# Kernel optimization log

Hardware: AMD Instinct MI355X
Metric: run time of the kernel (lower is better)

The kernel has to match this reference:

```python
import jax, jax.numpy as jnp
import numpy as np

B, D, L, H = 512, 512, 32, 300  # batch, input_dim, latent_dim, hidden_dim


def setup_inputs() -> dict:
    key = jax.random.key(0)
    ks = jax.random.split(key, 16)
    s = lambda k, *sh: jax.random.normal(k, sh, dtype=jnp.float32) * 0.05
    return {
        "x": jax.random.normal(ks[0], (B, D), dtype=jnp.float32),
        "eps": jax.random.normal(ks[1], (B, L), dtype=jnp.float32),
        "W": jax.random.normal(ks[2], (D, L), dtype=jnp.float32),  # mask (get_generator_mask -> W)
        "qz_w1": s(ks[3], D, H), "qz_b1": s(ks[4], H),
        "qz_w2": s(ks[5], H, H), "qz_b2": s(ks[6], H),
        "zm_w": s(ks[7], H, L), "zm_b": s(ks[8], L),
        "zl_w": s(ks[9], H, L), "zl_b": s(ks[10], L),
        "gen_w1": s(ks[11], L, H),               # no bias (bias=False)
        "gen_w2": s(ks[12], H, H), "gen_b2": s(ks[13], H),
        "col_w": s(ks[14], D, H), "col_b": s(ks[15], D),  # stacked column_means Linears
    }


def reference(x, eps, W, qz_w1, qz_b1, qz_w2, qz_b2, zm_w, zm_b, zl_w, zl_b,
              gen_w1, gen_w2, gen_b2, col_w, col_b):
    # encode
    h = jax.nn.relu(x @ qz_w1 + qz_b1)
    h = jax.nn.relu(h @ qz_w2 + qz_b2)
    z_mean = h @ zm_w + zm_b
    z_log_var = h @ zl_w + zl_b
    # reparameterize (eps supplied as input)
    z = z_mean + eps * jnp.exp(0.5 * z_log_var)
    # decode: per-column masked generator MLP, batched over columns j
    masked = W[:, None, :] * z[None, :, :]                 # [D, B, L]
    g = jax.nn.relu(jnp.einsum('jbl,lh->jbh', masked, gen_w1))
    g = jax.nn.relu(jnp.einsum('jbh,hk->jbk', g, gen_w2) + gen_b2)
    x_rec = jnp.einsum('jbh,jh->jb', g, col_w) + col_b[:, None]  # [D, B]
    x_mean = x_rec.T                                       # [B, D]
    return (x_mean, z, z_mean, z_log_var)
```

## Files before the change

### kernel.cpp

```cpp
#include <hip/hip_runtime.h>

#define B_ 512
#define D_ 512
#define L_ 32
#define H_ 300
#define NT 19
#define NS 10
#define G1S 308

typedef unsigned short ushort_t;
typedef __bf16 bf16x8 __attribute__((ext_vector_type(8)));
typedef float f32x4 __attribute__((ext_vector_type(4)));

union B8 { ushort_t u[8]; uint4 q; bf16x8 v; uint2 d[2]; __bf16 b[8]; };

__device__ __forceinline__ void split8(const float* fv, B8& hi, B8& lo) {
    #pragma unroll
    for (int i = 0; i < 8; ++i) {
        __bf16 h = (__bf16)fv[i];
        hi.b[i] = h;
        lo.b[i] = (__bf16)(fv[i] - (float)h);
    }
}

__global__ __launch_bounds__(64) void prep_kernel(
        const float* __restrict__ gw1, const float* __restrict__ gw2,
        const float* __restrict__ qw1, const float* __restrict__ qw2,
        const float* __restrict__ zmw, const float* __restrict__ zlw,
        ushort_t* __restrict__ gw1f, ushort_t* __restrict__ gw2f,
        ushort_t* __restrict__ w1hi, ushort_t* __restrict__ w1lo,
        ushort_t* __restrict__ w2hi, ushort_t* __restrict__ w2lo,
        ushort_t* __restrict__ w3hi, ushort_t* __restrict__ w3lo) {
    int blk = blockIdx.x;
    int l = threadIdx.x, grp = l >> 4, li = l & 15;
    if (blk < 209) {
        const float* src; int K, nt, s; ushort_t* dst;
        if (blk < 19) { nt = blk; s = 0; src = gw1; K = 32; dst = gw1f + (nt * 64 + l) * 8; }
        else { int i = blk - 19; nt = i / 10; s = i % 10; src = gw2; K = 300;
               dst = gw2f + ((nt * 10 + s) * 64 + l) * 8; }
        int n = nt * 16 + li;
        B8 V;
        #pragma unroll
        for (int i = 0; i < 8; ++i) {
            int k = 32 * s + 8 * grp + i;
            V.b[i] = (__bf16)((k < K && n < H_) ? src[k * H_ + n] : 0.f);
        }
        *reinterpret_cast<uint4*>(dst) = V.q;
    } else {
        const float* src = nullptr; int K, N, nt, s, stacked = 0;
        ushort_t *dh, *dl;
        if (blk < 513)      { int i = blk - 209; nt = i / 16; s = i % 16; src = qw1; K = 512; N = 300;
                              dh = w1hi + ((nt * 16 + s) * 64 + l) * 8; dl = w1lo + ((nt * 16 + s) * 64 + l) * 8; }
        else if (blk < 703) { int i = blk - 513; nt = i / 10; s = i % 10; src = qw2; K = 300; N = 300;
                              dh = w2hi + ((nt * 10 + s) * 64 + l) * 8; dl = w2lo + ((nt * 10 + s) * 64 + l) * 8; }
        else                { int i = blk - 703; nt = i / 10; s = i % 10; K = 300; N = 64; stacked = 1;
                              dh = w3hi + ((nt * 10 + s) * 64 + l) * 8; dl = w3lo + ((nt * 10 + s) * 64 + l) * 8; }
        int n = nt * 16 + li;
        float fv[8];
        #pragma unroll
        for (int i = 0; i < 8; ++i) {
            int k = 32 * s + 8 * grp + i;
            float v = 0.f;
            if (k < K && n < N) {
                if (!stacked) v = src[k * N + n];
                else          v = (n < 32) ? zmw[k * 32 + n] : zlw[k * 32 + (n - 32)];
            }
            fv[i] = v;
        }
        B8 Vh, Vl;
        split8(fv, Vh, Vl);
        *reinterpret_cast<uint4*>(dh) = Vh.q;
        *reinterpret_cast<uint4*>(dl) = Vl.q;
    }
}

template<int KSTEPS, bool RELU>
__global__ __launch_bounds__(256) void enc_gemm_f32(const float* __restrict__ A, int lda,
        const ushort_t* __restrict__ Whi, const ushort_t* __restrict__ Wlo,
        const float* __restrict__ bias, float* __restrict__ out, int ldo,
        int Ncols, int ntiles) {
    const int tid = threadIdx.x;
    const int w = tid >> 6, lane = tid & 63;
    const int grp = lane >> 4, li = lane & 15;
    const int r0 = blockIdx.x * 16;
    const int nt = blockIdx.y * 4 + w;
    const bool active = nt < ntiles;

    f32x4 acc = {0.f, 0.f, 0.f, 0.f};
    for (int s = 0; s < KSTEPS; ++s) {
        int kb = 32 * s + 8 * grp;
        B8 Ah, Al;
        if (kb + 8 <= lda) {
            const float* ap = A + (size_t)(r0 + li) * lda + kb;
            float4 f0 = *reinterpret_cast<const float4*>(ap);
            float4 f1 = *reinterpret_cast<const float4*>(ap + 4);
            float fv[8] = {f0.x, f0.y, f0.z, f0.w, f1.x, f1.y, f1.z, f1.w};
            split8(fv, Ah, Al);
        } else {
            Ah.q = make_uint4(0, 0, 0, 0);
            Al.q = make_uint4(0, 0, 0, 0);
        }
        if (active) {
            bf16x8 bh = *reinterpret_cast<const bf16x8*>(
                Whi + ((size_t)(nt * KSTEPS + s) * 64 + lane) * 8);
            bf16x8 bl = *reinterpret_cast<const bf16x8*>(
                Wlo + ((size_t)(nt * KSTEPS + s) * 64 + lane) * 8);
            acc = __builtin_amdgcn_mfma_f32_16x16x32_bf16(Ah.v, bh, acc, 0, 0, 0);
            acc = __builtin_amdgcn_mfma_f32_16x16x32_bf16(Al.v, bh, acc, 0, 0, 0);
            acc = __builtin_amdgcn_mfma_f32_16x16x32_bf16(Ah.v, bl, acc, 0, 0, 0);
        }
    }
    if (active) {
        int h = nt * 16 + li;
        float bv = (bias != nullptr && h < Ncols) ? bias[h] : 0.f;
        #pragma unroll
        for (int r = 0; r < 4; ++r) {
            float v = acc[r] + bv;
            if (RELU) v = fmaxf(v, 0.f);
            if (h >= Ncols) v = 0.f;
            out[(size_t)(r0 + 4 * grp + r) * ldo + h] = v;
        }
    }
}

__global__ __launch_bounds__(256) void enc3_reparam(const float* __restrict__ h2,
        const ushort_t* __restrict__ w3hi, const ushort_t* __restrict__ w3lo,
        const float* __restrict__ zmb, const float* __restrict__ zlb,
        const float* __restrict__ eps, float* __restrict__ out, float* __restrict__ zb) {
    __shared__ float zs[16][64];
    const int tid = threadIdx.x;
    const int w = tid >> 6, lane = tid & 63;
    const int grp = lane >> 4, li = lane & 15;
    const int r0 = blockIdx.x * 16;

    f32x4 acc = {0.f, 0.f, 0.f, 0.f};
    for (int s = 0; s < 10; ++s) {
        int kb = 32 * s + 8 * grp;
        B8 Ah, Al;
        if (kb + 8 <= 304) {
            const float* ap = h2 + (size_t)(r0 + li) * 304 + kb;
            float4 f0 = *reinterpret_cast<const float4*>(ap);
            float4 f1 = *reinterpret_cast<const float4*>(ap + 4);
            float fv[8] = {f0.x, f0.y, f0.z, f0.w, f1.x, f1.y, f1.z, f1.w};
            split8(fv, Ah, Al);
        } else {
            Ah.q = make_uint4(0, 0, 0, 0);
            Al.q = make_uint4(0, 0, 0, 0);
        }
        bf16x8 bh = *reinterpret_cast<const bf16x8*>(w3hi + ((size_t)(w * 10 + s) * 64 + lane) * 8);
        bf16x8 bl = *reinterpret_cast<const bf16x8*>(w3lo + ((size_t)(w * 10 + s) * 64 + lane) * 8);
        acc = __builtin_amdgcn_mfma_f32_16x16x32_bf16(Ah.v, bh, acc, 0, 0, 0);
        acc = __builtin_amdgcn_mfma_f32_16x16x32_bf16(Al.v, bh, acc, 0, 0, 0);
        acc = __builtin_amdgcn_mfma_f32_16x16x32_bf16(Ah.v, bl, acc, 0, 0, 0);
    }
    #pragma unroll
    for (int r = 0; r < 4; ++r) zs[4 * grp + r][w * 16 + li] = acc[r];
    __syncthreads();

    for (int idx = tid; idx < 512; idx += 256) {
        int m = idx >> 5, l2 = idx & 31;
        int row = r0 + m;
        float zm = zs[m][l2] + zmb[l2];
        float zl = zs[m][32 + l2] + zlb[l2];
        float zv = zm + eps[row * 32 + l2] * expf(0.5f * zl);
        out[B_ * D_ + row * 32 + l2] = zv;
        out[B_ * D_ + B_ * L_ + row * 32 + l2] = zm;
        out[B_ * D_ + 2 * B_ * L_ + row * 32 + l2] = zl;
        zb[row * 32 + l2] = zv;
    }
}

__global__ __launch_bounds__(512, 4) void decode_kernel(
        const float* __restrict__ z, const float* __restrict__ Wmask,
        const ushort_t* __restrict__ gw1f, const ushort_t* __restrict__ gw2f,
        const float* __restrict__ gb2, const float* __restrict__ colw,
        const float* __restrict__ colb, float* __restrict__ xmean) {
    __shared__ __align__(16) ushort_t g1s[64 * G1S + 16];
    __shared__ float xpart[8][64];

    const int j    = blockIdx.y;
    const int b0   = blockIdx.x * 64;
    const int tid  = threadIdx.x;
    const int w    = tid >> 6;
    const int lane = tid & 63;
    const int grp  = lane >> 4, li = lane & 15;
    const int ntl  = (w < 3) ? 3 : 2;

    B8 bm[4];
    {
        const float* wp = Wmask + (size_t)j * L_ + 8 * grp;
        float4 w0 = *reinterpret_cast<const float4*>(wp);
        float4 w1 = *reinterpret_cast<const float4*>(wp + 4);
        float wv[8] = {w0.x, w0.y, w0.z, w0.w, w1.x, w1.y, w1.z, w1.w};
        #pragma unroll
        for (int mt = 0; mt < 4; ++mt) {
            const float* zp = z + (size_t)(b0 + mt * 16 + li) * L_ + 8 * grp;
            float4 z0 = *reinterpret_cast<const float4*>(zp);
            float4 z1 = *reinterpret_cast<const float4*>(zp + 4);
            float zv[8] = {z0.x, z0.y, z0.z, z0.w, z1.x, z1.y, z1.z, z1.w};
            #pragma unroll
            for (int i = 0; i < 8; ++i) bm[mt].b[i] = (__bf16)(wv[i] * zv[i]);
        }
        if (tid < 272) {
            if (tid < 256) g1s[(tid >> 2) * G1S + 304 + (tid & 3)] = 0;
            else           g1s[64 * G1S + (tid - 256)] = 0;
        }
    }
    __syncthreads();

    #pragma unroll
    for (int t = 0; t < 3; ++t) {
        if (t < ntl) {
            int nt = w + 8 * t;
            bf16x8 ga = *reinterpret_cast<const bf16x8*>(gw1f + (nt * 64 + lane) * 8);
            #pragma unroll
            for (int mt = 0; mt < 4; ++mt) {
                f32x4 c = {0.f, 0.f, 0.f, 0.f};
                c = __builtin_amdgcn_mfma_f32_16x16x32_bf16(ga, bm[mt].v, c, 0, 0, 0);
                B8 P;
                #pragma unroll
                for (int r = 0; r < 4; ++r) P.b[r] = (__bf16)fmaxf(c[r], 0.f);
                *reinterpret_cast<uint2*>(&g1s[(mt * 16 + li) * G1S + nt * 16 + 4 * grp]) = P.d[0];
            }
        }
    }
    __syncthreads();

    {
        f32x4 acc[4][3];
        #pragma unroll
        for (int mt = 0; mt < 4; ++mt)
            #pragma unroll
            for (int t = 0; t < 3; ++t) acc[mt][t] = {0.f, 0.f, 0.f, 0.f};

        #pragma unroll 2
        for (int s = 0; s < NS; ++s) {
            B8 af[4];
            #pragma unroll
            for (int mt = 0; mt < 4; ++mt) {
                const ushort_t* p = &g1s[(mt * 16 + li) * G1S + 32 * s + 8 * grp];
                af[mt].d[0] = *reinterpret_cast<const uint2*>(p);
                af[mt].d[1] = *reinterpret_cast<const uint2*>(p + 4);
            }
            #pragma unroll
            for (int t = 0; t < 3; ++t) {
                if (t < ntl) {
                    int nt = w + 8 * t;
                    bf16x8 bfr = *reinterpret_cast<const bf16x8*>(
                        gw2f + ((size_t)(nt * NS + s) * 64 + lane) * 8);
                    #pragma unroll
                    for (int mt = 0; mt < 4; ++mt)
                        acc[mt][t] = __builtin_amdgcn_mfma_f32_16x16x32_bf16(
                            af[mt].v, bfr, acc[mt][t], 0, 0, 0);
                }
            }
        }

        float partial[4][4] = {};
        #pragma unroll
        for (int t = 0; t < 3; ++t) {
            if (t < ntl) {
                int h = (w + 8 * t) * 16 + li;
                float bias = 0.f, fac = 0.f;
                if (h < H_) { bias = gb2[h]; fac = colw[j * H_ + h]; }
                #pragma unroll
                for (int mt = 0; mt < 4; ++mt)
                    #pragma unroll
                    for (int r = 0; r < 4; ++r)
                        partial[mt][r] += fmaxf(acc[mt][t][r] + bias, 0.f) * fac;
            }
        }
        #pragma unroll
        for (int mt = 0; mt < 4; ++mt)
            #pragma unroll
            for (int r = 0; r < 4; ++r) {
                float v = partial[mt][r];
                v += __shfl_xor(v, 1);
                v += __shfl_xor(v, 2);
                v += __shfl_xor(v, 4);
                v += __shfl_xor(v, 8);
                if (li == 0) xpart[w][mt * 16 + 4 * grp + r] = v;
            }
    }
    __syncthreads();

    if (tid < 64) {
        float v = colb[j];
        #pragma unroll
        for (int ww = 0; ww < 8; ++ww) v += xpart[ww][tid];
        xmean[(size_t)(b0 + tid) * D_ + j] = v;
    }
}

extern "C" void kernel_launch(void* const* d_in, const int* in_sizes, int n_in,
                              void* d_out, int out_size, void* d_ws, size_t ws_size,
                              hipStream_t stream) {
    const float* x     = (const float*)d_in[0];
    const float* eps   = (const float*)d_in[1];
    const float* Wm    = (const float*)d_in[2];
    const float* qz_w1 = (const float*)d_in[3];
    const float* qz_b1 = (const float*)d_in[4];
    const float* qz_w2 = (const float*)d_in[5];
    const float* qz_b2 = (const float*)d_in[6];
    const float* zm_w  = (const float*)d_in[7];
    const float* zm_b  = (const float*)d_in[8];
    const float* zl_w  = (const float*)d_in[9];
    const float* zl_b  = (const float*)d_in[10];
    const float* gw1   = (const float*)d_in[11];
    const float* gw2   = (const float*)d_in[12];
    const float* gb2   = (const float*)d_in[13];
    const float* colw  = (const float*)d_in[14];
    const float* colb  = (const float*)d_in[15];
    float* out = (float*)d_out;
    char* ws = (char*)d_ws;

    ushort_t* gw1f = (ushort_t*)(ws + 0);
    ushort_t* gw2f = (ushort_t*)(ws + 19456);
    ushort_t* w1hi = (ushort_t*)(ws + 214016);
    ushort_t* w1lo = (ushort_t*)(ws + 525312);
    ushort_t* w2hi = (ushort_t*)(ws + 836608);
    ushort_t* w2lo = (ushort_t*)(ws + 1031168);
    ushort_t* w3hi = (ushort_t*)(ws + 1225728);
    ushort_t* w3lo = (ushort_t*)(ws + 1266688);
    float*    h1   = (float*)(ws + 1307648);
    float*    h2   = (float*)(ws + 214016);
    float*    zb   = (float*)(ws + 1930240);

    prep_kernel<<<743, 64, 0, stream>>>(gw1, gw2, qz_w1, qz_w2, zm_w, zl_w,
                                        gw1f, gw2f, w1hi, w1lo, w2hi, w2lo, w3hi, w3lo);
    enc_gemm_f32<16, true><<<dim3(32, 5), 256, 0, stream>>>(
        x, 512, w1hi, w1lo, qz_b1, h1, 304, 300, NT);
    enc_gemm_f32<10, true><<<dim3(32, 5), 256, 0, stream>>>(
        h1, 304, w2hi, w2lo, qz_b2, h2, 304, 300, NT);
    enc3_reparam<<<32, 256, 0, stream>>>(h2, w3hi, w3lo, zm_b, zl_b, eps, out, zb);
    decode_kernel<<<dim3(8, 512), 512, 0, stream>>>(zb, Wm, gw1f, gw2f, gb2, colw, colb, out);
}
```

Baseline: 127.2 us.

## Use 4 waves per decode block, each owning 5 contiguous N-tiles

The decode kernel drops from 8 to 4 waves per block. Each wave now handles 4-5 contiguous 16-wide hidden tiles instead of 2-3 strided ones, so each A fragment loaded from LDS feeds more MFMAs and LDS read traffic per MFMA falls. In exchange there is more accumulator register pressure (20 f32x4 accumulators) and less parallelism per block, and the launch bounds change to 256 threads with 3 blocks minimum.

```diff
diff --git a/kernel.cpp b/kernel.cpp
--- a/kernel.cpp
+++ b/kernel.cpp
@@ -170,13 +170,13 @@
     }
 }
 
-__global__ __launch_bounds__(512, 4) void decode_kernel(
+__global__ __launch_bounds__(256, 3) void decode_kernel(
         const float* __restrict__ z, const float* __restrict__ Wmask,
         const ushort_t* __restrict__ gw1f, const ushort_t* __restrict__ gw2f,
         const float* __restrict__ gb2, const float* __restrict__ colw,
         const float* __restrict__ colb, float* __restrict__ xmean) {
     __shared__ __align__(16) ushort_t g1s[64 * G1S + 16];
-    __shared__ float xpart[8][64];
+    __shared__ float xpart[4][64];
 
     const int j    = blockIdx.y;
     const int b0   = blockIdx.x * 64;
@@ -184,7 +184,7 @@
     const int w    = tid >> 6;
     const int lane = tid & 63;
     const int grp  = lane >> 4, li = lane & 15;
-    const int ntl  = (w < 3) ? 3 : 2;
+    const int nlocal = (w == 3) ? 4 : 5;
 
     B8 bm[4];
     {
@@ -201,17 +201,17 @@
             #pragma unroll
             for (int i = 0; i < 8; ++i) bm[mt].b[i] = (__bf16)(wv[i] * zv[i]);
         }
-        if (tid < 272) {
-            if (tid < 256) g1s[(tid >> 2) * G1S + 304 + (tid & 3)] = 0;
-            else           g1s[64 * G1S + (tid - 256)] = 0;
+        for (int idx = tid; idx < 272; idx += 256) {
+            if (idx < 256) g1s[(idx >> 2) * G1S + 304 + (idx & 3)] = 0;
+            else           g1s[64 * G1S + (idx - 256)] = 0;
         }
     }
     __syncthreads();
 
     #pragma unroll
-    for (int t = 0; t < 3; ++t) {
-        if (t < ntl) {
-            int nt = w + 8 * t;
+    for (int ntl = 0; ntl < 5; ++ntl) {
+        if (ntl < nlocal) {
+            int nt = w * 5 + ntl;
             bf16x8 ga = *reinterpret_cast<const bf16x8*>(gw1f + (nt * 64 + lane) * 8);
             #pragma unroll
             for (int mt = 0; mt < 4; ++mt) {
@@ -227,13 +227,13 @@
     __syncthreads();
 
     {
-        f32x4 acc[4][3];
+        f32x4 acc[4][5];
         #pragma unroll
         for (int mt = 0; mt < 4; ++mt)
             #pragma unroll
-            for (int t = 0; t < 3; ++t) acc[mt][t] = {0.f, 0.f, 0.f, 0.f};
-
-        #pragma unroll 2
+            for (int n = 0; n < 5; ++n) acc[mt][n] = {0.f, 0.f, 0.f, 0.f};
+
+        const size_t lane8 = (size_t)lane * 8;
         for (int s = 0; s < NS; ++s) {
             B8 af[4];
             #pragma unroll
@@ -243,31 +243,30 @@
                 af[mt].d[1] = *reinterpret_cast<const uint2*>(p + 4);
             }
             #pragma unroll
-            for (int t = 0; t < 3; ++t) {
-                if (t < ntl) {
-                    int nt = w + 8 * t;
+            for (int ntl = 0; ntl < 5; ++ntl) {
+                if (ntl < nlocal) {
                     bf16x8 bfr = *reinterpret_cast<const bf16x8*>(
-                        gw2f + ((size_t)(nt * NS + s) * 64 + lane) * 8);
+                        gw2f + (size_t)((w * 5 + ntl) * NS + s) * 512 + lane8);
                     #pragma unroll
                     for (int mt = 0; mt < 4; ++mt)
-                        acc[mt][t] = __builtin_amdgcn_mfma_f32_16x16x32_bf16(
-                            af[mt].v, bfr, acc[mt][t], 0, 0, 0);
+                        acc[mt][ntl] = __builtin_amdgcn_mfma_f32_16x16x32_bf16(
+                            af[mt].v, bfr, acc[mt][ntl], 0, 0, 0);
                 }
             }
         }
 
         float partial[4][4] = {};
         #pragma unroll
-        for (int t = 0; t < 3; ++t) {
-            if (t < ntl) {
-                int h = (w + 8 * t) * 16 + li;
+        for (int ntl = 0; ntl < 5; ++ntl) {
+            if (ntl < nlocal) {
+                int h = (w * 5 + ntl) * 16 + li;
                 float bias = 0.f, fac = 0.f;
                 if (h < H_) { bias = gb2[h]; fac = colw[j * H_ + h]; }
                 #pragma unroll
                 for (int mt = 0; mt < 4; ++mt)
                     #pragma unroll
                     for (int r = 0; r < 4; ++r)
-                        partial[mt][r] += fmaxf(acc[mt][t][r] + bias, 0.f) * fac;
+                        partial[mt][r] += fmaxf(acc[mt][ntl][r] + bias, 0.f) * fac;
             }
         }
         #pragma unroll
@@ -287,7 +286,7 @@
     if (tid < 64) {
         float v = colb[j];
         #pragma unroll
-        for (int ww = 0; ww < 8; ++ww) v += xpart[ww][tid];
+        for (int ww = 0; ww < 4; ++ww) v += xpart[ww][tid];
         xmean[(size_t)(b0 + tid) * D_ + j] = v;
     }
 }
@@ -333,5 +332,5 @@
     enc_gemm_f32<10, true><<<dim3(32, 5), 256, 0, stream>>>(
         h1, 304, w2hi, w2lo, qz_b2, h2, 304, 300, NT);
     enc3_reparam<<<32, 256, 0, stream>>>(h2, w3hi, w3lo, zm_b, zl_b, eps, out, zb);
-    decode_kernel<<<dim3(8, 512), 512, 0, stream>>>(zb, Wm, gw1f, gw2f, gb2, colw, colb, out);
-}
+    decode_kernel<<<dim3(8, 512), 256, 0, stream>>>(zb, Wm, gw1f, gw2f, gb2, colw, colb, out);
+}
```

Measured after the change: 111.9 us (median of 2 runs). -12.0%, faster.

## Make decode kernel persistent with gen_w2 fragments held in registers

Applied to the files above, without the earlier changes.

The decode kernel becomes persistent. It launches 256 blocks, and each block loops over 16 (column, batch-tile) units instead of one block per unit. Each wave loads its contiguous slice of gen_w1/gen_w2 bf16 fragments into registers once and reuses them for every unit, which removes the repeated global/L2 weight loads. The cost is heavy register use (launch bounds relaxed to 2 blocks per SM), fewer blocks in flight, and serialized units with syncs inside each block.

```diff
diff --git a/kernel.cpp b/kernel.cpp
--- a/kernel.cpp
+++ b/kernel.cpp
@@ -170,7 +170,7 @@
     }
 }
 
-__global__ __launch_bounds__(512, 4) void decode_kernel(
+__global__ __launch_bounds__(512, 2) void decode_kernel(
         const float* __restrict__ z, const float* __restrict__ Wmask,
         const ushort_t* __restrict__ gw1f, const ushort_t* __restrict__ gw2f,
         const float* __restrict__ gb2, const float* __restrict__ colw,
@@ -178,96 +178,118 @@
     __shared__ __align__(16) ushort_t g1s[64 * G1S + 16];
     __shared__ float xpart[8][64];
 
-    const int j    = blockIdx.y;
-    const int b0   = blockIdx.x * 64;
     const int tid  = threadIdx.x;
     const int w    = tid >> 6;
     const int lane = tid & 63;
     const int grp  = lane >> 4, li = lane & 15;
-    const int ntl  = (w < 3) ? 3 : 2;
-
-    B8 bm[4];
-    {
-        const float* wp = Wmask + (size_t)j * L_ + 8 * grp;
-        float4 w0 = *reinterpret_cast<const float4*>(wp);
-        float4 w1 = *reinterpret_cast<const float4*>(wp + 4);
-        float wv[8] = {w0.x, w0.y, w0.z, w0.w, w1.x, w1.y, w1.z, w1.w};
-        #pragma unroll
-        for (int mt = 0; mt < 4; ++mt) {
-            const float* zp = z + (size_t)(b0 + mt * 16 + li) * L_ + 8 * grp;
-            float4 z0 = *reinterpret_cast<const float4*>(zp);
-            float4 z1 = *reinterpret_cast<const float4*>(zp + 4);
-            float zv[8] = {z0.x, z0.y, z0.z, z0.w, z1.x, z1.y, z1.z, z1.w};
-            #pragma unroll
-            for (int i = 0; i < 8; ++i) bm[mt].b[i] = (__bf16)(wv[i] * zv[i]);
-        }
-        if (tid < 272) {
-            if (tid < 256) g1s[(tid >> 2) * G1S + 304 + (tid & 3)] = 0;
-            else           g1s[64 * G1S + (tid - 256)] = 0;
-        }
-    }
-    __syncthreads();
-
+    const int nlocal = (w < 3) ? 3 : 2;
+    const int nbeg   = (w < 3) ? w * 3 : 9 + (w - 3) * 2;
+
+    B8 breg[3][10];
     #pragma unroll
-    for (int t = 0; t < 3; ++t) {
-        if (t < ntl) {
-            int nt = w + 8 * t;
-            bf16x8 ga = *reinterpret_cast<const bf16x8*>(gw1f + (nt * 64 + lane) * 8);
+    for (int ntl = 0; ntl < 3; ++ntl) {
+        if (ntl < nlocal) {
+            #pragma unroll
+            for (int s = 0; s < NS; ++s)
+                breg[ntl][s].q = *reinterpret_cast<const uint4*>(
+                    gw2f + ((size_t)((nbeg + ntl) * NS + s) * 64 + lane) * 8);
+        }
+    }
+    B8 ga[3];
+    #pragma unroll
+    for (int ntl = 0; ntl < 3; ++ntl)
+        if (ntl < nlocal)
+            ga[ntl].q = *reinterpret_cast<const uint4*>(gw1f + ((nbeg + ntl) * 64 + lane) * 8);
+
+    if (tid < 272) {
+        if (tid < 256) g1s[(tid >> 2) * G1S + 304 + (tid & 3)] = 0;
+        else           g1s[64 * G1S + (tid - 256)] = 0;
+    }
+
+    const int base = blockIdx.x * 16;
+    for (int u = 0; u < 16; ++u) {
+        const int unit = base + u;
+        const int j  = unit >> 3;
+        const int b0 = (unit & 7) * 64;
+
+        B8 bm[4];
+        {
+            const float* wp = Wmask + (size_t)j * L_ + 8 * grp;
+            float4 w0 = *reinterpret_cast<const float4*>(wp);
+            float4 w1 = *reinterpret_cast<const float4*>(wp + 4);
+            float wv[8] = {w0.x, w0.y, w0.z, w0.w, w1.x, w1.y, w1.z, w1.w};
             #pragma unroll
             for (int mt = 0; mt < 4; ++mt) {
-                f32x4 c = {0.f, 0.f, 0.f, 0.f};
-                c = __builtin_amdgcn_mfma_f32_16x16x32_bf16(ga, bm[mt].v, c, 0, 0, 0);
-                B8 P;
+                const float* zp = z + (size_t)(b0 + mt * 16 + li) * L_ + 8 * grp;
+                float4 z0 = *reinterpret_cast<const float4*>(zp);
+                float4 z1 = *reinterpret_cast<const float4*>(zp + 4);
+                float zv[8] = {z0.x, z0.y, z0.z, z0.w, z1.x, z1.y, z1.z, z1.w};
                 #pragma unroll
-                for (int r = 0; r < 4; ++r) P.b[r] = (__bf16)fmaxf(c[r], 0.f);
-                *reinterpret_cast<uint2*>(&g1s[(mt * 16 + li) * G1S + nt * 16 + 4 * grp]) = P.d[0];
-            }
-        }
-    }
-    __syncthreads();
-
-    {
-        f32x4 acc[4][3];
-        #pragma unroll
-        for (int mt = 0; mt < 4; ++mt)
-            #pragma unroll
-            for (int t = 0; t < 3; ++t) acc[mt][t] = {0.f, 0.f, 0.f, 0.f};
-
-        #pragma unroll 2
-        for (int s = 0; s < NS; ++s) {
-            B8 af[4];
-            #pragma unroll
-            for (int mt = 0; mt < 4; ++mt) {
-                const ushort_t* p = &g1s[(mt * 16 + li) * G1S + 32 * s + 8 * grp];
-                af[mt].d[0] = *reinterpret_cast<const uint2*>(p);
-                af[mt].d[1] = *reinterpret_cast<const uint2*>(p + 4);
-            }
-            #pragma unroll
-            for (int t = 0; t < 3; ++t) {
-                if (t < ntl) {
-                    int nt = w + 8 * t;
-                    bf16x8 bfr = *reinterpret_cast<const bf16x8*>(
-                        gw2f + ((size_t)(nt * NS + s) * 64 + lane) * 8);
+                for (int i = 0; i < 8; ++i) bm[mt].b[i] = (__bf16)(wv[i] * zv[i]);
+            }
+        }
+        __syncthreads();
+
+        {
+            ushort_t* st = &g1s[li * G1S + 4 * grp];
+            #pragma unroll
+            for (int ntl = 0; ntl < 3; ++ntl) {
+                if (ntl < nlocal) {
+                    int nt = nbeg + ntl;
+                    #pragma unroll
+                    for (int mt = 0; mt < 4; ++mt) {
+                        f32x4 c = {0.f, 0.f, 0.f, 0.f};
+                        c = __builtin_amdgcn_mfma_f32_16x16x32_bf16(ga[ntl].v, bm[mt].v, c, 0, 0, 0);
+                        B8 P;
+                        #pragma unroll
+                        for (int r = 0; r < 4; ++r) P.b[r] = (__bf16)fmaxf(c[r], 0.f);
+                        *reinterpret_cast<uint2*>(st + mt * 16 * G1S + nt * 16) = P.d[0];
+                    }
+                }
+            }
+        }
+        __syncthreads();
+
+        float partial[4][4] = {};
+        {
+            f32x4 acc[4][3];
+            #pragma unroll
+            for (int mt = 0; mt < 4; ++mt)
+                #pragma unroll
+                for (int n = 0; n < 3; ++n) acc[mt][n] = {0.f, 0.f, 0.f, 0.f};
+
+            const ushort_t* ld = &g1s[li * G1S + 8 * grp];
+            #pragma unroll
+            for (int s = 0; s < NS; ++s) {
+                B8 af[4];
+                #pragma unroll
+                for (int mt = 0; mt < 4; ++mt) {
+                    af[mt].d[0] = *reinterpret_cast<const uint2*>(ld + mt * 16 * G1S + 32 * s);
+                    af[mt].d[1] = *reinterpret_cast<const uint2*>(ld + mt * 16 * G1S + 32 * s + 4);
+                }
+                #pragma unroll
+                for (int ntl = 0; ntl < 3; ++ntl) {
+                    if (ntl < nlocal) {
+                        #pragma unroll
+                        for (int mt = 0; mt < 4; ++mt)
+                            acc[mt][ntl] = __builtin_amdgcn_mfma_f32_16x16x32_bf16(
+                                af[mt].v, breg[ntl][s].v, acc[mt][ntl], 0, 0, 0);
+                    }
+                }
+            }
+
+            #pragma unroll
+            for (int ntl = 0; ntl < 3; ++ntl) {
+                if (ntl < nlocal) {
+                    int h = (nbeg + ntl) * 16 + li;
+                    float bias = 0.f, fac = 0.f;
+                    if (h < H_) { bias = gb2[h]; fac = colw[j * H_ + h]; }
                     #pragma unroll
                     for (int mt = 0; mt < 4; ++mt)
-                        acc[mt][t] = __builtin_amdgcn_mfma_f32_16x16x32_bf16(
-                            af[mt].v, bfr, acc[mt][t], 0, 0, 0);
+                        #pragma unroll
+                        for (int r = 0; r < 4; ++r)
+                            partial[mt][r] += fmaxf(acc[mt][ntl][r] + bias, 0.f) * fac;
                 }
-            }
-        }
-
-        float partial[4][4] = {};
-        #pragma unroll
-        for (int t = 0; t < 3; ++t) {
-            if (t < ntl) {
-                int h = (w + 8 * t) * 16 + li;
-                float bias = 0.f, fac = 0.f;
-                if (h < H_) { bias = gb2[h]; fac = colw[j * H_ + h]; }
-                #pragma unroll
-                for (int mt = 0; mt < 4; ++mt)
-                    #pragma unroll
-                    for (int r = 0; r < 4; ++r)
-                        partial[mt][r] += fmaxf(acc[mt][t][r] + bias, 0.f) * fac;
             }
         }
         #pragma unroll
@@ -281,14 +303,14 @@
                 v += __shfl_xor(v, 8);
                 if (li == 0) xpart[w][mt * 16 + 4 * grp + r] = v;
             }
-    }
-    __syncthreads();
-
-    if (tid < 64) {
-        float v = colb[j];
-        #pragma unroll
-        for (int ww = 0; ww < 8; ++ww) v += xpart[ww][tid];
-        xmean[(size_t)(b0 + tid) * D_ + j] = v;
+        __syncthreads();
+
+        if (tid < 64) {
+            float v = colb[j];
+            #pragma unroll
+            for (int ww = 0; ww < 8; ++ww) v += xpart[ww][tid];
+            xmean[(size_t)(b0 + tid) * D_ + j] = v;
+        }
     }
 }
 
@@ -333,5 +355,5 @@
     enc_gemm_f32<10, true><<<dim3(32, 5), 256, 0, stream>>>(
         h1, 304, w2hi, w2lo, qz_b2, h2, 304, 300, NT);
     enc3_reparam<<<32, 256, 0, stream>>>(h2, w3hi, w3lo, zm_b, zl_b, eps, out, zb);
-    decode_kernel<<<dim3(8, 512), 512, 0, stream>>>(zb, Wm, gw1f, gw2f, gb2, colw, colb, out);
-}
+    decode_kernel<<<256, 512, 0, stream>>>(zb, Wm, gw1f, gw2f, gb2, colw, colb, out);
+}
```

New measurement: 143.2 us. +12.5%, slower.
